# Performance work log

Hardware: AMD Instinct MI355X
Metric: run time of the kernel (lower is better)

## Reference

```python
import jax, jax.numpy as jnp
import numpy as np

INPUT_DIM = 1024
HIDDEN_DIM = 2048
NUM_BLOCKS = 8
BLOCK_SIZE = HIDDEN_DIM // NUM_BLOCKS
BATCH = 2048


def setup_inputs() -> dict:
    key = jax.random.key(0)
    ks = jax.random.split(key, 6)
    # PyTorch GRUCell init: uniform(-1/sqrt(hidden_size), 1/sqrt(hidden_size))
    bound = 1.0 / np.sqrt(BLOCK_SIZE)
    u = lambda k, shape: jax.random.uniform(k, shape, jnp.float32, -bound, bound)
    return {
        "input": jax.random.normal(ks[0], (BATCH, INPUT_DIM), jnp.float32),
        "hidden": jax.random.normal(ks[1], (BATCH, HIDDEN_DIM), jnp.float32),
        # stacked per-block GRUCell params (block-diagonal structure)
        "W_ih": u(ks[2], (NUM_BLOCKS, 3 * BLOCK_SIZE, INPUT_DIM)),
        "W_hh": u(ks[3], (NUM_BLOCKS, 3 * BLOCK_SIZE, BLOCK_SIZE)),
        "b_ih": u(ks[4], (NUM_BLOCKS, 3 * BLOCK_SIZE)),
        "b_hh": u(ks[5], (NUM_BLOCKS, 3 * BLOCK_SIZE)),
    }


def reference(input, hidden, W_ih, W_hh, b_ih, b_hh):
    B = input.shape[0]
    nb, g3, bs = W_hh.shape  # [num_blocks, 3*block_size, block_size]
    hb = hidden.reshape(B, nb, bs)                      # [B, nb, bs]
    # input-to-gate and hidden-to-gate projections, batched over blocks
    gi = jnp.einsum("bi,ngi->bng", input, W_ih) + b_ih  # [B, nb, 3*bs]
    gh = jnp.einsum("bns,ngs->bng", hb, W_hh) + b_hh    # [B, nb, 3*bs]
    i_r, i_z, i_n = jnp.split(gi, 3, axis=-1)
    h_r, h_z, h_n = jnp.split(gh, 3, axis=-1)
    r = jax.nn.sigmoid(i_r + h_r)
    z = jax.nn.sigmoid(i_z + h_z)
    n = jnp.tanh(i_n + r * h_n)
    new_h = (1.0 - z) * n + z * hb                      # [B, nb, bs]
    return new_h.reshape(B, nb * bs)
```

## Files before the change

### kernel.cpp

```cpp
#include <hip/hip_runtime.h>
#include <hip/hip_bf16.h>
#include <type_traits>

#define AS1 __attribute__((address_space(1)))
#define AS3 __attribute__((address_space(3)))

typedef __attribute__((ext_vector_type(4))) float f32x4;
typedef __attribute__((ext_vector_type(8))) short bf16x8;

static constexpr int B_   = 2048;
static constexpr int IN_  = 1024;
static constexpr int HID_ = 2048;
static constexpr int NB_  = 8;
static constexpr int BS_  = 256;
static constexpr int G3_  = 768;

__device__ __forceinline__ unsigned short f2bf(float f) {
  unsigned u = __builtin_bit_cast(unsigned, f);
  u = (u + 0x7FFFu + ((u >> 16) & 1u)) >> 16;
  return (unsigned short)u;
}

__global__ void cvt_all(const float* __restrict__ x, const float* __restrict__ h,
                        const float* __restrict__ Wih, const float* __restrict__ Whh,
                        unsigned short* __restrict__ dst) {
  constexpr int c0 = (B_ * IN_) / 4;
  constexpr int c1 = c0 + (B_ * HID_) / 4;
  constexpr int c2 = c1 + (NB_ * G3_ * IN_) / 4;
  constexpr int n4 = c2 + (NB_ * G3_ * BS_) / 4;
  int i = blockIdx.x * blockDim.x + threadIdx.x;
  int stride = gridDim.x * blockDim.x;
  for (; i < n4; i += stride) {
    float4 v;
    if (i < c0)       v = reinterpret_cast<const float4*>(x)[i];
    else if (i < c1)  v = reinterpret_cast<const float4*>(h)[i - c0];
    else if (i < c2)  v = reinterpret_cast<const float4*>(Wih)[i - c1];
    else              v = reinterpret_cast<const float4*>(Whh)[i - c2];
    ushort4 o;
    o.x = f2bf(v.x); o.y = f2bf(v.y); o.z = f2bf(v.z); o.w = f2bf(v.w);
    reinterpret_cast<ushort4*>(dst)[i] = o;
  }
}

__global__ __launch_bounds__(256, 2) void gru_mfma(
    const unsigned short* __restrict__ inb,
    const unsigned short* __restrict__ hidb,
    const unsigned short* __restrict__ wihb,
    const unsigned short* __restrict__ whhb,
    const float* __restrict__ hid_f32,
    const float* __restrict__ b_ih,
    const float* __restrict__ b_hh,
    float* __restrict__ out)
{
  __shared__ __align__(16) char lds[2][40960];

  const int t    = threadIdx.x;
  const int lane = t & 63;
  const int wid  = t >> 6;
  const int wm   = wid >> 1;
  const int wn   = wid & 1;

  const int bid = blockIdx.x;
  const int swz = (bid & 7) * 64 + (bid >> 3);
  const int mt  = swz & 15;
  const int ct  = swz >> 4;
  const int mrow0 = mt * 128;
  const int n     = ct >> 2;
  const int s0    = (ct & 3) * 64;

  int arow[4], acb[4];
#pragma unroll
  for (int p = 0; p < 4; ++p) {
    int op = p * 4096 + t * 16;
    int ol = op ^ (((op >> 7) & 7) << 4);
    arow[p] = ol >> 7; acb[p] = ol & 127;
  }
  int wrowg[6], wsl[6], wcb[6];
#pragma unroll
  for (int p = 0; p < 6; ++p) {
    int op = p * 4096 + t * 16;
    int ol = op ^ (((op >> 7) & 7) << 4);
    int wr = ol >> 7;
    wrowg[p] = wr >> 6;
    wsl[p]   = wr & 63;
    wcb[p]   = ol & 127;
  }

  f32x4 acc[4][4][2] = {};

  auto stage = [&](int buf, int t2) {
    const bool ph1 = t2 < 16;
    const int ks = ph1 ? t2 : (t2 - 16);
    char* base = (char*)lds[buf];
#pragma unroll
    for (int p = 0; p < 4; ++p) {
      const char* src = ph1
        ? (const char*)inb  + ((size_t)(mrow0 + arow[p]) * IN_  + ks * 64) * 2 + acb[p]
        : (const char*)hidb + ((size_t)(mrow0 + arow[p]) * HID_ + n * BS_ + ks * 64) * 2 + acb[p];
      __builtin_amdgcn_global_load_lds((const AS1 void*)src,
                                       (AS3 void*)(base + p * 4096 + wid * 1024), 16, 0, 0);
    }
#pragma unroll
    for (int p = 0; p < 6; ++p) {
      int grow = n * G3_ + wrowg[p] * BS_ + s0 + wsl[p];
      const char* src = ph1
        ? (const char*)wihb + ((size_t)grow * IN_ + ks * 64) * 2 + wcb[p]
        : (const char*)whhb + ((size_t)grow * BS_ + ks * 64) * 2 + wcb[p];
      __builtin_amdgcn_global_load_lds((const AS1 void*)src,
                                       (AS3 void*)(base + 16384 + p * 4096 + wid * 1024), 16, 0, 0);
    }
  };

  auto compute = [&](int buf, auto ph1c) {
    constexpr bool PH1 = decltype(ph1c)::value;
    const char* Ab = (const char*)lds[buf];
    const char* Wb = (const char*)lds[buf] + 16384;
#pragma unroll
    for (int ksub = 0; ksub < 2; ++ksub) {
      bf16x8 af[4];
#pragma unroll
      for (int mi = 0; mi < 4; ++mi) {
        int ar  = wm * 64 + mi * 16 + (lane & 15);
        int off = ar * 128 + ksub * 64 + ((lane >> 4) * 16);
        off ^= (ar & 7) << 4;
        af[mi] = *reinterpret_cast<const bf16x8*>(Ab + off);
      }
#pragma unroll
      for (int g = 0; g < 3; ++g) {
        bf16x8 wf[2];
#pragma unroll
        for (int ni = 0; ni < 2; ++ni) {
          int wr  = g * 64 + wn * 32 + ni * 16 + (lane & 15);
          int off = wr * 128 + ksub * 64 + ((lane >> 4) * 16);
          off ^= (wr & 7) << 4;
          wf[ni] = *reinterpret_cast<const bf16x8*>(Wb + off);
        }
        constexpr int set2 = PH1 ? 2 : 3;
        const int set = (g < 2) ? g : set2;
#pragma unroll
        for (int mi = 0; mi < 4; ++mi)
#pragma unroll
          for (int ni = 0; ni < 2; ++ni)
            acc[set][mi][ni] = __builtin_amdgcn_mfma_f32_16x16x32_bf16(
                af[mi], wf[ni], acc[set][mi][ni], 0, 0, 0);
      }
    }
  };

  stage(0, 0);
  stage(1, 1);
#pragma unroll
  for (int tt = 0; tt < 20; ++tt) {
    const int cur = tt & 1;
    __builtin_amdgcn_sched_barrier(0);
    if (tt < 19) asm volatile("s_waitcnt vmcnt(10)");
    else         asm volatile("s_waitcnt vmcnt(0)");
    __builtin_amdgcn_sched_barrier(0);
    __builtin_amdgcn_s_barrier();
    if (tt < 16) compute(cur, std::true_type{});
    else         compute(cur, std::false_type{});
    asm volatile("s_waitcnt lgkmcnt(0)");
    __builtin_amdgcn_sched_barrier(0);
    __builtin_amdgcn_s_barrier();
    if (tt + 2 < 20) stage(cur, tt + 2);
  }

#pragma unroll
  for (int ni = 0; ni < 2; ++ni) {
    int scol = s0 + wn * 32 + ni * 16 + (lane & 15);
    float br_i = b_ih[n * G3_ + 0 * BS_ + scol];
    float bz_i = b_ih[n * G3_ + 1 * BS_ + scol];
    float bn_i = b_ih[n * G3_ + 2 * BS_ + scol];
    float br_h = b_hh[n * G3_ + 0 * BS_ + scol];
    float bz_h = b_hh[n * G3_ + 1 * BS_ + scol];
    float bn_h = b_hh[n * G3_ + 2 * BS_ + scol];
    int gcol = n * BS_ + scol;
#pragma unroll
    for (int mi = 0; mi < 4; ++mi) {
#pragma unroll
      for (int i = 0; i < 4; ++i) {
        int row = mrow0 + wm * 64 + mi * 16 + (lane >> 4) * 4 + i;
        float hprev = hid_f32[(size_t)row * HID_ + gcol];
        float rr = acc[0][mi][ni][i] + br_i + br_h;
        float zz = acc[1][mi][ni][i] + bz_i + bz_h;
        float r  = 1.f / (1.f + __expf(-rr));
        float z  = 1.f / (1.f + __expf(-zz));
        float ng = tanhf(acc[2][mi][ni][i] + bn_i + r * (acc[3][mi][ni][i] + bn_h));
        out[(size_t)row * HID_ + gcol] = (1.f - z) * ng + z * hprev;
      }
    }
  }
}

__global__ void gru_naive(const float* __restrict__ x, const float* __restrict__ h,
                          const float* __restrict__ Wih, const float* __restrict__ Whh,
                          const float* __restrict__ bih, const float* __restrict__ bhh,
                          float* __restrict__ out) {
  int b = blockIdx.x;
  int n = blockIdx.y;
  int s = threadIdx.x;
  __shared__ float xs[1024];
  __shared__ float hs[256];
  for (int i = threadIdx.x; i < 1024; i += 256) xs[i] = x[(size_t)b * IN_ + i];
  if (threadIdx.x < 256) hs[threadIdx.x] = h[(size_t)b * HID_ + n * BS_ + threadIdx.x];
  __syncthreads();
  float gi[3], gh[3];
  for (int g = 0; g < 3; ++g) {
    const float* w = Wih + ((size_t)(n * G3_ + g * BS_ + s)) * IN_;
    float a = 0.f;
    for (int k = 0; k < IN_; ++k) a += xs[k] * w[k];
    gi[g] = a + bih[n * G3_ + g * BS_ + s];
    const float* w2 = Whh + ((size_t)(n * G3_ + g * BS_ + s)) * BS_;
    float a2 = 0.f;
    for (int k = 0; k < BS_; ++k) a2 += hs[k] * w2[k];
    gh[g] = a2 + bhh[n * G3_ + g * BS_ + s];
  }
  float r = 1.f / (1.f + expf(-(gi[0] + gh[0])));
  float z = 1.f / (1.f + expf(-(gi[1] + gh[1])));
  float ng = tanhf(gi[2] + r * gh[2]);
  out[(size_t)b * HID_ + n * BS_ + s] = (1.f - z) * ng + z * hs[s];
}

extern "C" void kernel_launch(void* const* d_in, const int* in_sizes, int n_in,
                              void* d_out, int out_size, void* d_ws, size_t ws_size,
                              hipStream_t stream) {
  const float* x   = (const float*)d_in[0];
  const float* h   = (const float*)d_in[1];
  const float* Wih = (const float*)d_in[2];
  const float* Whh = (const float*)d_in[3];
  const float* bih = (const float*)d_in[4];
  const float* bhh = (const float*)d_in[5];
  float* out = (float*)d_out;

  const size_t szin  = (size_t)B_ * IN_;
  const size_t szhid = (size_t)B_ * HID_;
  const size_t szwih = (size_t)NB_ * G3_ * IN_;
  const size_t szwhh = (size_t)NB_ * G3_ * BS_;
  const size_t need  = (szin + szhid + szwih + szwhh) * 2;

  if (ws_size >= need) {
    unsigned short* inb  = (unsigned short*)d_ws;
    unsigned short* hidb = inb + szin;
    unsigned short* wihb = hidb + szhid;
    unsigned short* whhb = wihb + szwih;
    cvt_all<<<2048, 256, 0, stream>>>(x, h, Wih, Whh, (unsigned short*)d_ws);
    gru_mfma<<<512, 256, 0, stream>>>(inb, hidb, wihb, whhb, h, bih, bhh, out);
  } else {
    dim3 grid(B_, NB_);
    gru_naive<<<grid, 256, 0, stream>>>(x, h, Wih, Whh, bih, bhh, out);
  }
}
```

Baseline: 57.27 us.

## Split main loop into per-gate phases interleaving global-to-LDS staging with MFMA

Restructures the double-buffered GEMM loop so each K-step is split into three gate phases. Each phase loads LDS fragments, issues a slice of the next tiles' global-to-LDS loads, then runs its MFMAs at raised wave priority (s_setprio). The intent is to spread memory issue across compute, in a ping-pong style, rather than bursting all loads after compute. This adds more barriers per iteration and relies on delicate vmcnt accounting, so an error there could race on LDS or stall.

```diff
diff --git a/kernel.cpp b/kernel.cpp
--- a/kernel.cpp
+++ b/kernel.cpp
@@ -7,6 +7,8 @@
 
 typedef __attribute__((ext_vector_type(4))) float f32x4;
 typedef __attribute__((ext_vector_type(8))) short bf16x8;
+
+template <int V> using ic = std::integral_constant<int, V>;
 
 static constexpr int B_   = 2048;
 static constexpr int IN_  = 1024;
@@ -88,81 +90,108 @@
 
   f32x4 acc[4][4][2] = {};
 
-  auto stage = [&](int buf, int t2) {
+  auto stage = [&](int buf, int t2, int from, int to) {
     const bool ph1 = t2 < 16;
     const int ks = ph1 ? t2 : (t2 - 16);
     char* base = (char*)lds[buf];
 #pragma unroll
-    for (int p = 0; p < 4; ++p) {
-      const char* src = ph1
-        ? (const char*)inb  + ((size_t)(mrow0 + arow[p]) * IN_  + ks * 64) * 2 + acb[p]
-        : (const char*)hidb + ((size_t)(mrow0 + arow[p]) * HID_ + n * BS_ + ks * 64) * 2 + acb[p];
-      __builtin_amdgcn_global_load_lds((const AS1 void*)src,
-                                       (AS3 void*)(base + p * 4096 + wid * 1024), 16, 0, 0);
+    for (int p = 0; p < 10; ++p) {
+      if (p < from || p >= to) continue;
+      if (p < 4) {
+        const char* src = ph1
+          ? (const char*)inb  + ((size_t)(mrow0 + arow[p]) * IN_  + ks * 64) * 2 + acb[p]
+          : (const char*)hidb + ((size_t)(mrow0 + arow[p]) * HID_ + n * BS_ + ks * 64) * 2 + acb[p];
+        __builtin_amdgcn_global_load_lds((const AS1 void*)src,
+                                         (AS3 void*)(base + p * 4096 + wid * 1024), 16, 0, 0);
+      } else {
+        const int q = p - 4;
+        int grow = n * G3_ + wrowg[q] * BS_ + s0 + wsl[q];
+        const char* src = ph1
+          ? (const char*)wihb + ((size_t)grow * IN_ + ks * 64) * 2 + wcb[q]
+          : (const char*)whhb + ((size_t)grow * BS_ + ks * 64) * 2 + wcb[q];
+        __builtin_amdgcn_global_load_lds((const AS1 void*)src,
+                                         (AS3 void*)(base + 16384 + q * 4096 + wid * 1024), 16, 0, 0);
+      }
     }
-#pragma unroll
-    for (int p = 0; p < 6; ++p) {
-      int grow = n * G3_ + wrowg[p] * BS_ + s0 + wsl[p];
-      const char* src = ph1
-        ? (const char*)wihb + ((size_t)grow * IN_ + ks * 64) * 2 + wcb[p]
-        : (const char*)whhb + ((size_t)grow * BS_ + ks * 64) * 2 + wcb[p];
-      __builtin_amdgcn_global_load_lds((const AS1 void*)src,
-                                       (AS3 void*)(base + 16384 + p * 4096 + wid * 1024), 16, 0, 0);
-    }
-  };
-
-  auto compute = [&](int buf, auto ph1c) {
-    constexpr bool PH1 = decltype(ph1c)::value;
-    const char* Ab = (const char*)lds[buf];
-    const char* Wb = (const char*)lds[buf] + 16384;
-#pragma unroll
-    for (int ksub = 0; ksub < 2; ++ksub) {
-      bf16x8 af[4];
+  };
+
+  auto loadA = [&](int buf, bf16x8 (&af)[2][4]) {
+#pragma unroll
+    for (int ksub = 0; ksub < 2; ++ksub)
 #pragma unroll
       for (int mi = 0; mi < 4; ++mi) {
         int ar  = wm * 64 + mi * 16 + (lane & 15);
         int off = ar * 128 + ksub * 64 + ((lane >> 4) * 16);
         off ^= (ar & 7) << 4;
-        af[mi] = *reinterpret_cast<const bf16x8*>(Ab + off);
-      }
-#pragma unroll
-      for (int g = 0; g < 3; ++g) {
-        bf16x8 wf[2];
-#pragma unroll
-        for (int ni = 0; ni < 2; ++ni) {
-          int wr  = g * 64 + wn * 32 + ni * 16 + (lane & 15);
-          int off = wr * 128 + ksub * 64 + ((lane >> 4) * 16);
-          off ^= (wr & 7) << 4;
-          wf[ni] = *reinterpret_cast<const bf16x8*>(Wb + off);
-        }
-        constexpr int set2 = PH1 ? 2 : 3;
-        const int set = (g < 2) ? g : set2;
-#pragma unroll
-        for (int mi = 0; mi < 4; ++mi)
-#pragma unroll
-          for (int ni = 0; ni < 2; ++ni)
-            acc[set][mi][ni] = __builtin_amdgcn_mfma_f32_16x16x32_bf16(
-                af[mi], wf[ni], acc[set][mi][ni], 0, 0, 0);
-      }
-    }
-  };
-
-  stage(0, 0);
-  stage(1, 1);
+        af[ksub][mi] = *reinterpret_cast<const bf16x8*>((const char*)lds[buf] + off);
+      }
+  };
+  auto loadW = [&](int buf, int g, bf16x8 (&wf)[2][2]) {
+#pragma unroll
+    for (int ksub = 0; ksub < 2; ++ksub)
+#pragma unroll
+      for (int ni = 0; ni < 2; ++ni) {
+        int wr  = g * 64 + wn * 32 + ni * 16 + (lane & 15);
+        int off = wr * 128 + ksub * 64 + ((lane >> 4) * 16);
+        off ^= (wr & 7) << 4;
+        wf[ksub][ni] = *reinterpret_cast<const bf16x8*>((const char*)lds[buf] + 16384 + off);
+      }
+  };
+  auto mfmaSet = [&](auto setc, bf16x8 (&af)[2][4], bf16x8 (&wf)[2][2]) {
+    constexpr int set = decltype(setc)::value;
+    __builtin_amdgcn_s_setprio(1);
+#pragma unroll
+    for (int ksub = 0; ksub < 2; ++ksub)
+#pragma unroll
+      for (int mi = 0; mi < 4; ++mi)
+#pragma unroll
+        for (int ni = 0; ni < 2; ++ni)
+          acc[set][mi][ni] = __builtin_amdgcn_mfma_f32_16x16x32_bf16(
+              af[ksub][mi], wf[ksub][ni], acc[set][mi][ni], 0, 0, 0);
+    __builtin_amdgcn_s_setprio(0);
+  };
+
+  stage(0, 0, 0, 10);
+  stage(1, 1, 0, 8);
+  __builtin_amdgcn_sched_barrier(0);
+  asm volatile("s_waitcnt vmcnt(8)");
+  __builtin_amdgcn_sched_barrier(0);
+  __builtin_amdgcn_s_barrier();
+
 #pragma unroll
   for (int tt = 0; tt < 20; ++tt) {
-    const int cur = tt & 1;
-    __builtin_amdgcn_sched_barrier(0);
-    if (tt < 19) asm volatile("s_waitcnt vmcnt(10)");
-    else         asm volatile("s_waitcnt vmcnt(0)");
-    __builtin_amdgcn_sched_barrier(0);
-    __builtin_amdgcn_s_barrier();
-    if (tt < 16) compute(cur, std::true_type{});
-    else         compute(cur, std::false_type{});
+    const int cur = tt & 1, oth = cur ^ 1;
+    bf16x8 af[2][4], wf[2][2];
+
+    loadA(cur, af);
+    loadW(cur, 0, wf);
+    if (tt + 1 < 20) stage(oth, tt + 1, 8, 10);
+    __builtin_amdgcn_s_barrier();
     asm volatile("s_waitcnt lgkmcnt(0)");
     __builtin_amdgcn_sched_barrier(0);
-    __builtin_amdgcn_s_barrier();
-    if (tt + 2 < 20) stage(cur, tt + 2);
+    mfmaSet(ic<0>{}, af, wf);
+    __builtin_amdgcn_s_barrier();
+
+    loadW(cur, 1, wf);
+    if (tt + 2 < 20) stage(cur, tt + 2, 0, 6);
+    __builtin_amdgcn_s_barrier();
+    asm volatile("s_waitcnt lgkmcnt(0)");
+    __builtin_amdgcn_sched_barrier(0);
+    mfmaSet(ic<1>{}, af, wf);
+    __builtin_amdgcn_s_barrier();
+
+    loadW(cur, 2, wf);
+    if (tt + 2 < 20) stage(cur, tt + 2, 6, 8);
+    __builtin_amdgcn_sched_barrier(0);
+    if (tt <= 17)      asm volatile("s_waitcnt vmcnt(8)");
+    else if (tt == 18) asm volatile("s_waitcnt vmcnt(0)");
+    __builtin_amdgcn_sched_barrier(0);
+    __builtin_amdgcn_s_barrier();
+    asm volatile("s_waitcnt lgkmcnt(0)");
+    __builtin_amdgcn_sched_barrier(0);
+    if (tt < 16) mfmaSet(ic<2>{}, af, wf);
+    else         mfmaSet(ic<3>{}, af, wf);
+    __builtin_amdgcn_s_barrier();
   }
 
 #pragma unroll
```

Measured after the change: 56.89 us. No clear change (-0.7%).
